# Kernel tuning notes

Measured on AMD Instinct MI355X. Metric: run time of the kernel, lower is better.

## Reference

```python
import jax, jax.numpy as jnp
import numpy as np

T, B, I, H = 512, 64, 512, 512

def setup_inputs() -> dict:
    key = jax.random.key(0)
    ks = jax.random.split(key, 9)
    s = 1.0 / np.sqrt(I + H)
    return {
        "inputs": jax.random.normal(ks[0], (T, B, I), dtype=jnp.float32),
        "Wf": jax.random.normal(ks[1], (H, I + H), dtype=jnp.float32) * s,
        "bf": jax.random.normal(ks[2], (H,), dtype=jnp.float32) * s,
        "Wi": jax.random.normal(ks[3], (H, I + H), dtype=jnp.float32) * s,
        "bi": jax.random.normal(ks[4], (H,), dtype=jnp.float32) * s,
        "Wg": jax.random.normal(ks[5], (H, I + H), dtype=jnp.float32) * s,
        "bg": jax.random.normal(ks[6], (H,), dtype=jnp.float32) * s,
        "Wo": jax.random.normal(ks[7], (H, I + H), dtype=jnp.float32) * s,
        "bo": jax.random.normal(ks[8], (H,), dtype=jnp.float32) * s,
    }

def reference(inputs, Wf, bf, Wi, bi, Wg, bg, Wo, bo):
    # Stack the 4 gate linears into one GEMM per step: W_all [4H, I+H]
    W_all = jnp.concatenate([Wf, Wi, Wg, Wo], axis=0)
    b_all = jnp.concatenate([bf, bi, bg, bo], axis=0)
    h = inputs.shape[1], Wf.shape[0]
    hx0 = jnp.zeros((inputs.shape[1], Wf.shape[0]), dtype=inputs.dtype)
    cx0 = jnp.zeros_like(hx0)

    def step(carry, x):
        hx, cx = carry
        combined = jnp.concatenate([x, hx], axis=1)        # [B, I+H]
        gates = combined @ W_all.T + b_all                 # [B, 4H]
        f_raw, i_raw, g_raw, o_raw = jnp.split(gates, 4, axis=1)
        f = jax.nn.sigmoid(f_raw)
        i = jax.nn.sigmoid(i_raw)
        g = jnp.tanh(g_raw)
        o = jax.nn.sigmoid(o_raw)
        cx = f * cx + i * g
        hx = o * jnp.tanh(cx)
        return (hx, cx), hx

    (hx, cx), stacked = jax.lax.scan(step, (hx0, cx0), inputs)
    return stacked, hx, cx
```

## Files before the change

### kernel.cpp

```cpp
#include <hip/hip_runtime.h>
#include <hip/hip_bf16.h>
#include <stdint.h>

typedef __bf16 bf16_t;
typedef __bf16 bf16x8 __attribute__((ext_vector_type(8)));
typedef __bf16 bf16x4_t __attribute__((ext_vector_type(4)));
typedef float f32x4 __attribute__((ext_vector_type(4)));

#define T_STEPS 512
#define B_SZ 64
#define I_SZ 512
#define H_SZ 512
#define NB 4
#define BS 16
#define NC 32
#define CS 16

#define XBF_OFF   0ull
#define WBF_OFF   33554432ull
#define BALL_OFF  (WBF_OFF + 4194304ull)
#define HEXP_OFF  (BALL_OFF + 8192ull)

__device__ __forceinline__ float sigmoid_fast(float x) {
  return 1.f / (1.f + __expf(-x));
}
__device__ __forceinline__ float tanh_fast(float x) {
  float xc = fminf(fmaxf(x, -10.f), 10.f);
  float e = __expf(2.f * xc);
  return (e - 1.f) / (e + 1.f);
}

__device__ __forceinline__ uint4 load_b128_cc(const void* addr) {
  uint4 v;
  asm volatile("global_load_dwordx4 %0, %1, off sc0 sc1"
               : "=v"(v) : "v"(addr) : "memory");
  return v;
}
__device__ __forceinline__ void store_b32_cc(void* addr, uint32_t v) {
  asm volatile("global_store_dword %0, %1, off sc0 sc1"
               :: "v"(addr), "v"(v) : "memory");
}
__device__ __forceinline__ void wait_vm0() {
  asm volatile("s_waitcnt vmcnt(0)" ::: "memory");
}

__global__ void prep_x(const float* __restrict__ x, bf16_t* __restrict__ xbf) {
  const int nch = (T_STEPS * B_SZ * I_SZ) / 8;
  int c = blockIdx.x * blockDim.x + threadIdx.x;
  int stride = gridDim.x * blockDim.x;
  for (; c < nch; c += stride) {
    int lane = c & 63;
    int kt = (c >> 6) & 7;
    int w  = (c >> 9) & 1;
    int bg = (c >> 10) & 3;
    int t  = c >> 12;
    int r = lane & 15, quad = lane >> 4;
    const float* src = x + ((size_t)t * B_SZ + bg * BS + r) * I_SZ + w * 256 + kt * 32 + quad * 8;
    float4 lo = *(const float4*)src;
    float4 hi = *(const float4*)(src + 4);
    bf16x8 o = { (bf16_t)lo.x, (bf16_t)lo.y, (bf16_t)lo.z, (bf16_t)lo.w,
                 (bf16_t)hi.x, (bf16_t)hi.y, (bf16_t)hi.z, (bf16_t)hi.w };
    *(bf16x8*)(xbf + (size_t)c * 8) = o;
  }
}

__global__ void prep_rest(const float* __restrict__ wf, const float* __restrict__ wi,
                          const float* __restrict__ wgm, const float* __restrict__ wo,
                          const float* __restrict__ bfv, const float* __restrict__ biv,
                          const float* __restrict__ bgv, const float* __restrict__ bov,
                          bf16_t* __restrict__ wbf, float* __restrict__ ball,
                          uint32_t* __restrict__ hexp) {
  int gtid = blockIdx.x * blockDim.x + threadIdx.x;
  int stride = gridDim.x * blockDim.x;
  const int WCH = (2048 * 1024) / 4;
  for (int i = gtid; i < WCH; i += stride) {
    int r = i >> 8;
    int c = (i & 255) << 2;
    int g = r >> 9, sr = r & 511;
    const float* src = (g == 0) ? wf : (g == 1) ? wi : (g == 2) ? wgm : wo;
    float4 v = *(const float4*)(src + (size_t)sr * 1024 + c);
    bf16x4_t o = { (bf16_t)v.x, (bf16_t)v.y, (bf16_t)v.z, (bf16_t)v.w };
    *(bf16x4_t*)(wbf + (size_t)r * 1024 + c) = o;
  }
  for (int i = gtid; i < 2048; i += stride) {
    int g = i >> 9;
    const float* src = (g == 0) ? bfv : (g == 1) ? biv : (g == 2) ? bgv : bov;
    ball[i] = src[i & 511];
  }
  for (int i = gtid; i < 65536; i += stride) hexp[i] = 0;
}

__global__ __launch_bounds__(256, 1) void qlstm_main(
    const bf16_t* __restrict__ xbf, const bf16_t* __restrict__ wbf,
    const float* __restrict__ ball, uint32_t* __restrict__ hexp,
    float* __restrict__ out) {
  const int wg = blockIdx.x;
  const int bg = wg >> 5;
  const int ic = wg & 31;
  const int tid = threadIdx.x;
  const int wave = tid >> 6;
  const int lane = tid & 63;
  const int l15 = lane & 15;
  const int quad = lane >> 4;

  __shared__ __align__(16) float Gp[2][4][16][68];

  bf16x8 wfr[4][8];
#pragma unroll
  for (int g = 0; g < 4; ++g) {
    const bf16_t* wp = wbf + ((size_t)(g * 512 + ic * CS + l15)) * 1024 + wave * 256 + quad * 8;
#pragma unroll
    for (int kt = 0; kt < 8; ++kt) wfr[g][kt] = *(const bf16x8*)(wp + kt * 32);
  }

  const int erow = tid >> 4;
  const int ecol = tid & 15;
  const float bias_f = ball[0 * 512 + ic * CS + ecol];
  const float bias_i = ball[1 * 512 + ic * CS + ecol];
  const float bias_g = ball[2 * 512 + ic * CS + ecol];
  const float bias_o = ball[3 * 512 + ic * CS + ecol];

  const int brow = bg * BS + erow;
  const int hcol = ic * CS + ecol;

  const int wh = hcol >> 8;
  const int kp = hcol & 255;
  const int pof = wh * 4096 + ((kp >> 5) << 9) + ((((kp >> 3) & 3) * 16 + erow) << 3) + (kp & 7);
  const int cof = ((wave - 2) << 12) + (lane << 3);

  float c_state = 0.f, h = 0.f;
  const size_t out_hx = (size_t)T_STEPS * B_SZ * H_SZ;

  const bf16_t* xw0 = xbf + ((size_t)(bg * 2 + wave) << 12) + lane * 8;

#pragma unroll 1
  for (int t = 0; t < T_STEPS; ++t) {
    const int par = t & 1;

    bf16x8 f[8];
    if (wave < 2) {
      const bf16_t* xp = xw0 + ((size_t)t << 15);
#pragma unroll
      for (int kt = 0; kt < 8; ++kt) f[kt] = *(const bf16x8*)(xp + kt * 512);
    } else {
      const uint32_t* hp = hexp + ((size_t)(((par ^ 1) * 4 + bg) << 13)) + cof;
      uint4 v[16];
      const uint32_t pat = (uint32_t)t << 16;
      for (;;) {
#pragma unroll
        for (int kt = 0; kt < 8; ++kt) {
          v[2 * kt]     = load_b128_cc(hp + kt * 512);
          v[2 * kt + 1] = load_b128_cc(hp + kt * 512 + 4);
        }
        wait_vm0();
        uint32_t bad = 0;
#pragma unroll
        for (int q = 0; q < 16; ++q)
          bad |= (v[q].x ^ pat) | (v[q].y ^ pat) | (v[q].z ^ pat) | (v[q].w ^ pat);
        if (__all((int)((bad & 0xffff0000u) == 0))) break;
        __builtin_amdgcn_s_sleep(1);
      }
#pragma unroll
      for (int kt = 0; kt < 8; ++kt) {
        uint4 a = v[2 * kt], b = v[2 * kt + 1];
        union { uint32_t u[4]; bf16x8 fv; } cv;
        cv.u[0] = (a.x & 0xffffu) | (a.y << 16);
        cv.u[1] = (a.z & 0xffffu) | (a.w << 16);
        cv.u[2] = (b.x & 0xffffu) | (b.y << 16);
        cv.u[3] = (b.z & 0xffffu) | (b.w << 16);
        f[kt] = cv.fv;
      }
    }

    f32x4 a0 = {0, 0, 0, 0}, a1 = {0, 0, 0, 0}, a2 = {0, 0, 0, 0}, a3 = {0, 0, 0, 0};
#pragma unroll
    for (int kt = 0; kt < 8; ++kt) {
      a0 = __builtin_amdgcn_mfma_f32_16x16x32_bf16(f[kt], wfr[0][kt], a0, 0, 0, 0);
      a1 = __builtin_amdgcn_mfma_f32_16x16x32_bf16(f[kt], wfr[1][kt], a1, 0, 0, 0);
      a2 = __builtin_amdgcn_mfma_f32_16x16x32_bf16(f[kt], wfr[2][kt], a2, 0, 0, 0);
      a3 = __builtin_amdgcn_mfma_f32_16x16x32_bf16(f[kt], wfr[3][kt], a3, 0, 0, 0);
    }

#pragma unroll
    for (int i = 0; i < 4; ++i) {
      f32x4 pv = { a0[i], a1[i], a2[i], a3[i] };
      *(f32x4*)&Gp[par][wave][quad * 4 + i][l15 * 4] = pv;
    }
    __syncthreads();

    f32x4 s = *(const f32x4*)&Gp[par][0][erow][ecol * 4];
    s += *(const f32x4*)&Gp[par][1][erow][ecol * 4];
    s += *(const f32x4*)&Gp[par][2][erow][ecol * 4];
    s += *(const f32x4*)&Gp[par][3][erow][ecol * 4];

    float fg = sigmoid_fast(s[0] + bias_f);
    float ig = sigmoid_fast(s[1] + bias_i);
    float gg = tanh_fast(s[2] + bias_g);
    float og = sigmoid_fast(s[3] + bias_o);
    c_state = fg * c_state + ig * gg;
    h = og * tanh_fast(c_state);

    union { bf16_t b; unsigned short u; } cvt;
    cvt.b = (bf16_t)h;
    uint32_t pk = ((uint32_t)(t + 1) << 16) | (uint32_t)cvt.u;
    store_b32_cc(hexp + (((par * 4 + bg) << 13) + pof), pk);

    out[((size_t)t * B_SZ + brow) * H_SZ + hcol] = h;
  }

  out[out_hx + (size_t)brow * H_SZ + hcol] = h;
  out[out_hx + (size_t)(B_SZ * H_SZ) + (size_t)brow * H_SZ + hcol] = c_state;
}

extern "C" void kernel_launch(void* const* d_in, const int* in_sizes, int n_in,
                              void* d_out, int out_size, void* d_ws, size_t ws_size,
                              hipStream_t stream) {
  const float* x   = (const float*)d_in[0];
  const float* Wf  = (const float*)d_in[1];
  const float* bfv = (const float*)d_in[2];
  const float* Wi  = (const float*)d_in[3];
  const float* biv = (const float*)d_in[4];
  const float* Wg  = (const float*)d_in[5];
  const float* bgv = (const float*)d_in[6];
  const float* Wo  = (const float*)d_in[7];
  const float* bov = (const float*)d_in[8];
  float* out = (float*)d_out;

  char* ws = (char*)d_ws;
  bf16_t* xbf    = (bf16_t*)(ws + XBF_OFF);
  bf16_t* wbf    = (bf16_t*)(ws + WBF_OFF);
  float*  ball   = (float*)(ws + BALL_OFF);
  uint32_t* hexp = (uint32_t*)(ws + HEXP_OFF);

  prep_x<<<dim3(2048), dim3(256), 0, stream>>>(x, xbf);
  prep_rest<<<dim3(1024), dim3(256), 0, stream>>>(Wf, Wi, Wg, Wo, bfv, biv, bgv, bov,
                                                  wbf, ball, hexp);
  qlstm_main<<<dim3(NB * NC), dim3(256), 0, stream>>>(xbf, wbf, ball, hexp, out);
}
```

Before: 1.341 ms.

## Split K across all waves and overlap x-projection with h wait via counters

Each wave now handles a quarter of both the input and recurrent K range, instead of two waves doing only x and two only h. That lets every wave compute its x contribution before waiting on the previous step's h. A per-step atomic counter (one increment per wave per workgroup, 128 in total) acts as a cheap readiness flag before polling the tagged h buffer, and the tag check is kept as a retry loop that recomputes the MFMAs. The aim is to hide the x-GEMM behind inter-workgroup sync latency and spread polling load, at the cost of extra atomics and possible recomputation on retry.

```diff
diff --git a/kernel.cpp b/kernel.cpp
--- a/kernel.cpp
+++ b/kernel.cpp
@@ -15,11 +15,13 @@
 #define BS 16
 #define NC 32
 #define CS 16
+#define CNT_TARGET 128
 
 #define XBF_OFF   0ull
 #define WBF_OFF   33554432ull
 #define BALL_OFF  (WBF_OFF + 4194304ull)
 #define HEXP_OFF  (BALL_OFF + 8192ull)
+#define FLGC_OFF  (HEXP_OFF + 262144ull)
 
 __device__ __forceinline__ float sigmoid_fast(float x) {
   return 1.f / (1.f + __expf(-x));
@@ -69,7 +71,7 @@
                           const float* __restrict__ bfv, const float* __restrict__ biv,
                           const float* __restrict__ bgv, const float* __restrict__ bov,
                           bf16_t* __restrict__ wbf, float* __restrict__ ball,
-                          uint32_t* __restrict__ hexp) {
+                          uint32_t* __restrict__ hexp, uint32_t* __restrict__ flgc) {
   int gtid = blockIdx.x * blockDim.x + threadIdx.x;
   int stride = gridDim.x * blockDim.x;
   const int WCH = (2048 * 1024) / 4;
@@ -88,12 +90,13 @@
     ball[i] = src[i & 511];
   }
   for (int i = gtid; i < 65536; i += stride) hexp[i] = 0;
+  for (int i = gtid; i < NB * T_STEPS; i += stride) flgc[i] = 0;
 }
 
 __global__ __launch_bounds__(256, 1) void qlstm_main(
     const bf16_t* __restrict__ xbf, const bf16_t* __restrict__ wbf,
     const float* __restrict__ ball, uint32_t* __restrict__ hexp,
-    float* __restrict__ out) {
+    uint32_t* __restrict__ flgc, float* __restrict__ out) {
   const int wg = blockIdx.x;
   const int bg = wg >> 5;
   const int ic = wg & 31;
@@ -102,16 +105,25 @@
   const int lane = tid & 63;
   const int l15 = lane & 15;
   const int quad = lane >> 4;
+  const int kq = wave * 4;
 
   __shared__ __align__(16) float Gp[2][4][16][68];
 
   bf16x8 wfr[4][8];
 #pragma unroll
   for (int g = 0; g < 4; ++g) {
-    const bf16_t* wp = wbf + ((size_t)(g * 512 + ic * CS + l15)) * 1024 + wave * 256 + quad * 8;
-#pragma unroll
-    for (int kt = 0; kt < 8; ++kt) wfr[g][kt] = *(const bf16x8*)(wp + kt * 32);
-  }
+    const bf16_t* wp = wbf + ((size_t)(g * 512 + ic * CS + l15)) * 1024 + quad * 8;
+#pragma unroll
+    for (int j = 0; j < 4; ++j) {
+      wfr[g][j]     = *(const bf16x8*)(wp + (kq + j) * 32);
+      wfr[g][4 + j] = *(const bf16x8*)(wp + 512 + (kq + j) * 32);
+    }
+  }
+
+  int off[4];
+#pragma unroll
+  for (int j = 0; j < 4; ++j)
+    off[j] = (((kq + j) >> 3) << 12) + (((kq + j) & 7) << 9) + lane * 8;
 
   const int erow = tid >> 4;
   const int ecol = tid & 15;
@@ -126,60 +138,80 @@
   const int wh = hcol >> 8;
   const int kp = hcol & 255;
   const int pof = wh * 4096 + ((kp >> 5) << 9) + ((((kp >> 3) & 3) * 16 + erow) << 3) + (kp & 7);
-  const int cof = ((wave - 2) << 12) + (lane << 3);
 
   float c_state = 0.f, h = 0.f;
   const size_t out_hx = (size_t)T_STEPS * B_SZ * H_SZ;
 
-  const bf16_t* xw0 = xbf + ((size_t)(bg * 2 + wave) << 12) + lane * 8;
+  const bf16_t* xwb = xbf + ((size_t)bg << 13);
 
 #pragma unroll 1
   for (int t = 0; t < T_STEPS; ++t) {
     const int par = t & 1;
 
-    bf16x8 f[8];
-    if (wave < 2) {
-      const bf16_t* xp = xw0 + ((size_t)t << 15);
-#pragma unroll
-      for (int kt = 0; kt < 8; ++kt) f[kt] = *(const bf16x8*)(xp + kt * 512);
-    } else {
-      const uint32_t* hp = hexp + ((size_t)(((par ^ 1) * 4 + bg) << 13)) + cof;
-      uint4 v[16];
-      const uint32_t pat = (uint32_t)t << 16;
-      for (;;) {
-#pragma unroll
-        for (int kt = 0; kt < 8; ++kt) {
-          v[2 * kt]     = load_b128_cc(hp + kt * 512);
-          v[2 * kt + 1] = load_b128_cc(hp + kt * 512 + 4);
-        }
-        wait_vm0();
-        uint32_t bad = 0;
-#pragma unroll
-        for (int q = 0; q < 16; ++q)
-          bad |= (v[q].x ^ pat) | (v[q].y ^ pat) | (v[q].z ^ pat) | (v[q].w ^ pat);
-        if (__all((int)((bad & 0xffff0000u) == 0))) break;
-        __builtin_amdgcn_s_sleep(1);
+    const uint32_t* cp = flgc + bg * T_STEPS + (t > 0 ? t - 1 : 0);
+    uint32_t cval = CNT_TARGET;
+    if (t > 0)
+      cval = __hip_atomic_load(cp, __ATOMIC_RELAXED, __HIP_MEMORY_SCOPE_AGENT);
+
+    f32x4 x0 = {0, 0, 0, 0}, x1 = {0, 0, 0, 0}, x2 = {0, 0, 0, 0}, x3 = {0, 0, 0, 0};
+    {
+      const bf16_t* xp = xwb + ((size_t)t << 15);
+      bf16x8 fx0 = *(const bf16x8*)(xp + off[0]);
+      bf16x8 fx1 = *(const bf16x8*)(xp + off[1]);
+      bf16x8 fx2 = *(const bf16x8*)(xp + off[2]);
+      bf16x8 fx3 = *(const bf16x8*)(xp + off[3]);
+      x0 = __builtin_amdgcn_mfma_f32_16x16x32_bf16(fx0, wfr[0][0], x0, 0, 0, 0);
+      x1 = __builtin_amdgcn_mfma_f32_16x16x32_bf16(fx0, wfr[1][0], x1, 0, 0, 0);
+      x2 = __builtin_amdgcn_mfma_f32_16x16x32_bf16(fx0, wfr[2][0], x2, 0, 0, 0);
+      x3 = __builtin_amdgcn_mfma_f32_16x16x32_bf16(fx0, wfr[3][0], x3, 0, 0, 0);
+      x0 = __builtin_amdgcn_mfma_f32_16x16x32_bf16(fx1, wfr[0][1], x0, 0, 0, 0);
+      x1 = __builtin_amdgcn_mfma_f32_16x16x32_bf16(fx1, wfr[1][1], x1, 0, 0, 0);
+      x2 = __builtin_amdgcn_mfma_f32_16x16x32_bf16(fx1, wfr[2][1], x2, 0, 0, 0);
+      x3 = __builtin_amdgcn_mfma_f32_16x16x32_bf16(fx1, wfr[3][1], x3, 0, 0, 0);
+      x0 = __builtin_amdgcn_mfma_f32_16x16x32_bf16(fx2, wfr[0][2], x0, 0, 0, 0);
+      x1 = __builtin_amdgcn_mfma_f32_16x16x32_bf16(fx2, wfr[1][2], x1, 0, 0, 0);
+      x2 = __builtin_amdgcn_mfma_f32_16x16x32_bf16(fx2, wfr[2][2], x2, 0, 0, 0);
+      x3 = __builtin_amdgcn_mfma_f32_16x16x32_bf16(fx2, wfr[3][2], x3, 0, 0, 0);
+      x0 = __builtin_amdgcn_mfma_f32_16x16x32_bf16(fx3, wfr[0][3], x0, 0, 0, 0);
+      x1 = __builtin_amdgcn_mfma_f32_16x16x32_bf16(fx3, wfr[1][3], x1, 0, 0, 0);
+      x2 = __builtin_amdgcn_mfma_f32_16x16x32_bf16(fx3, wfr[2][3], x2, 0, 0, 0);
+      x3 = __builtin_amdgcn_mfma_f32_16x16x32_bf16(fx3, wfr[3][3], x3, 0, 0, 0);
+    }
+
+    while (cval < CNT_TARGET)
+      cval = __hip_atomic_load(cp, __ATOMIC_RELAXED, __HIP_MEMORY_SCOPE_AGENT);
+
+    const uint32_t* hb = hexp + ((size_t)(((par ^ 1) * 4 + bg)) << 13);
+    const uint32_t pat = (uint32_t)t << 16;
+    f32x4 a0, a1, a2, a3;
+    uint32_t bad;
+    do {
+      uint4 v[8];
+#pragma unroll
+      for (int j = 0; j < 4; ++j) {
+        v[2 * j]     = load_b128_cc(hb + off[j]);
+        v[2 * j + 1] = load_b128_cc(hb + off[j] + 4);
       }
-#pragma unroll
-      for (int kt = 0; kt < 8; ++kt) {
-        uint4 a = v[2 * kt], b = v[2 * kt + 1];
+      wait_vm0();
+      a0 = x0; a1 = x1; a2 = x2; a3 = x3;
+#pragma unroll
+      for (int j = 0; j < 4; ++j) {
+        uint4 a = v[2 * j], b = v[2 * j + 1];
         union { uint32_t u[4]; bf16x8 fv; } cv;
         cv.u[0] = (a.x & 0xffffu) | (a.y << 16);
         cv.u[1] = (a.z & 0xffffu) | (a.w << 16);
         cv.u[2] = (b.x & 0xffffu) | (b.y << 16);
         cv.u[3] = (b.z & 0xffffu) | (b.w << 16);
-        f[kt] = cv.fv;
+        a0 = __builtin_amdgcn_mfma_f32_16x16x32_bf16(cv.fv, wfr[0][4 + j], a0, 0, 0, 0);
+        a1 = __builtin_amdgcn_mfma_f32_16x16x32_bf16(cv.fv, wfr[1][4 + j], a1, 0, 0, 0);
+        a2 = __builtin_amdgcn_mfma_f32_16x16x32_bf16(cv.fv, wfr[2][4 + j], a2, 0, 0, 0);
+        a3 = __builtin_amdgcn_mfma_f32_16x16x32_bf16(cv.fv, wfr[3][4 + j], a3, 0, 0, 0);
       }
-    }
-
-    f32x4 a0 = {0, 0, 0, 0}, a1 = {0, 0, 0, 0}, a2 = {0, 0, 0, 0}, a3 = {0, 0, 0, 0};
-#pragma unroll
-    for (int kt = 0; kt < 8; ++kt) {
-      a0 = __builtin_amdgcn_mfma_f32_16x16x32_bf16(f[kt], wfr[0][kt], a0, 0, 0, 0);
-      a1 = __builtin_amdgcn_mfma_f32_16x16x32_bf16(f[kt], wfr[1][kt], a1, 0, 0, 0);
-      a2 = __builtin_amdgcn_mfma_f32_16x16x32_bf16(f[kt], wfr[2][kt], a2, 0, 0, 0);
-      a3 = __builtin_amdgcn_mfma_f32_16x16x32_bf16(f[kt], wfr[3][kt], a3, 0, 0, 0);
-    }
+      bad = 0;
+#pragma unroll
+      for (int q = 0; q < 8; ++q)
+        bad |= (v[q].x ^ pat) | (v[q].y ^ pat) | (v[q].z ^ pat) | (v[q].w ^ pat);
+    } while (!__all((int)((bad & 0xffff0000u) == 0)));
 
 #pragma unroll
     for (int i = 0; i < 4; ++i) {
@@ -203,7 +235,10 @@
     union { bf16_t b; unsigned short u; } cvt;
     cvt.b = (bf16_t)h;
     uint32_t pk = ((uint32_t)(t + 1) << 16) | (uint32_t)cvt.u;
-    store_b32_cc(hexp + (((par * 4 + bg) << 13) + pof), pk);
+    store_b32_cc(hexp + ((size_t)((par * 4 + bg)) << 13) + pof, pk);
+    if (lane == 0)
+      __hip_atomic_fetch_add(&flgc[bg * T_STEPS + t], 1u,
+                             __ATOMIC_RELAXED, __HIP_MEMORY_SCOPE_AGENT);
 
     out[((size_t)t * B_SZ + brow) * H_SZ + hcol] = h;
   }
@@ -231,9 +266,10 @@
   bf16_t* wbf    = (bf16_t*)(ws + WBF_OFF);
   float*  ball   = (float*)(ws + BALL_OFF);
   uint32_t* hexp = (uint32_t*)(ws + HEXP_OFF);
+  uint32_t* flgc = (uint32_t*)(ws + FLGC_OFF);
 
   prep_x<<<dim3(2048), dim3(256), 0, stream>>>(x, xbf);
   prep_rest<<<dim3(1024), dim3(256), 0, stream>>>(Wf, Wi, Wg, Wo, bfv, biv, bgv, bov,
-                                                  wbf, ball, hexp);
-  qlstm_main<<<dim3(NB * NC), dim3(256), 0, stream>>>(xbf, wbf, ball, hexp, out);
-}
+                                                  wbf, ball, hexp, flgc);
+  qlstm_main<<<dim3(NB * NC), dim3(256), 0, stream>>>(xbf, wbf, ball, hexp, flgc, out);
+}
```

After: 1.931 ms. +44.0%, slower.
